# Performance work log

Hardware: AMD Instinct MI355X
Metric: run time of the kernel (lower is better)

The kernel has to match this reference:

```python
import jax, jax.numpy as jnp
import numpy as np

N_NODES = 200000
N_BONDS = 220000
D = 128


def setup_inputs() -> dict:
    key = jax.random.key(0)
    ks = jax.random.split(key, 8)
    h = jax.random.normal(ks[0], (N_NODES, D), dtype=jnp.float32)
    src = jax.random.randint(ks[1], (N_BONDS,), 0, N_NODES, dtype=jnp.int64)
    dst = jax.random.randint(ks[2], (N_BONDS,), 0, N_NODES, dtype=jnp.int64)
    # MLP params (Sequential: Linear(256,128)+ReLU, Linear(128,128)+ReLU, Linear(128,2))
    W1 = jax.random.normal(ks[3], (2 * D, 128), dtype=jnp.float32) * (1.0 / np.sqrt(2 * D))
    b1 = jnp.zeros((128,), dtype=jnp.float32)
    W2 = jax.random.normal(ks[4], (128, 128), dtype=jnp.float32) * (1.0 / np.sqrt(128))
    b2 = jnp.zeros((128,), dtype=jnp.float32)
    W3 = jax.random.normal(ks[5], (128, 2), dtype=jnp.float32) * (1.0 / np.sqrt(128))
    b3 = jnp.zeros((2,), dtype=jnp.float32)
    return {"h": h, "src": src, "dst": dst,
            "W1": W1, "b1": b1, "W2": W2, "b2": b2, "W3": W3, "b3": b3}


def _mlp(x, W1, b1, W2, b2, W3, b3):
    x = jax.nn.relu(x @ W1 + b1)
    x = jax.nn.relu(x @ W2 + b2)
    return x @ W3 + b3


def reference(h, src, dst, W1, b1, W2, b2, W3, b3):
    # forward edges: (src -> dst); reverse edges: (dst -> src)
    h_src = h[src]            # [E, D] gather
    h_dst = h[dst]            # [E, D] gather
    h_forward = jnp.concatenate([h_src, h_dst], axis=1)  # [E, 2D]
    h_reverse = jnp.concatenate([h_dst, h_src], axis=1)  # [E, 2D]
    return (_mlp(h_forward, W1, b1, W2, b2, W3, b3)
            + _mlp(h_reverse, W1, b1, W2, b2, W3, b3))
```

## Files before the change

### kernel.cpp

```cpp
#include <hip/hip_runtime.h>
#include <hip/hip_bf16.h>
#include <stdint.h>


typedef __attribute__((ext_vector_type(8))) short bf16x8;
typedef __attribute__((ext_vector_type(4))) float f32x4;

__device__ __forceinline__ float bf2f(unsigned u16) {
    union { unsigned u; float f; } v; v.u = u16 << 16;
    return v.f;
}
__device__ __forceinline__ unsigned short f2bf(float f) {
    union { float f; unsigned u; } v; v.f = f;
    unsigned u = v.u;
    unsigned r = u + 0x7FFFu + ((u >> 16) & 1u);
    return (unsigned short)(r >> 16);
}

__device__ __forceinline__ int swz(int f, int c) {
    return f * 128 + ((c ^ (f & 7)) << 3);
}
__device__ __forceinline__ int swzA(int f, int c) {
    return f * 256 + ((c ^ (f & 7)) << 3);
}

__device__ __forceinline__ bf16x8 cvt8v(float4 x, float4 y) {
    union { bf16x8 v; __hip_bfloat162 h[4]; } R;
    R.h[0] = __float22bfloat162_rn(float2{x.x, x.y});
    R.h[1] = __float22bfloat162_rn(float2{x.z, x.w});
    R.h[2] = __float22bfloat162_rn(float2{y.x, y.y});
    R.h[3] = __float22bfloat162_rn(float2{y.z, y.w});
    return R.v;
}

#define MFMA(a, b, c) __builtin_amdgcn_mfma_f32_16x16x32_bf16((a), (b), (c), 0, 0, 0)

__global__ void prep_weights(const float* __restrict__ W1,
                             const float* __restrict__ W2,
                             unsigned short* __restrict__ W1c,
                             unsigned short* __restrict__ W2t) {
    int idx = blockIdx.x * 256 + threadIdx.x;
    if (idx < 128 * 256) {
        int j = idx >> 8, k = idx & 255;
        W1c[idx] = f2bf(W1[k * 128 + j]);
    } else {
        int i2 = idx - 128 * 256;
        if (i2 < 128 * 128) {
            int n = i2 >> 7, k = i2 & 127;
            W2t[i2] = f2bf(W2[k * 128 + n]);
        }
    }
}

__global__ __launch_bounds__(512, 1) void edge_fused(
    const float* __restrict__ h, const int* __restrict__ src,
    const int* __restrict__ dst, const unsigned short* __restrict__ W1c,
    const unsigned short* __restrict__ W2t, const float* __restrict__ b1,
    const float* __restrict__ b2, const float* __restrict__ W3,
    const float* __restrict__ b3, float* __restrict__ out, int E) {
    __shared__ unsigned short W1s[128 * 256];
    __shared__ unsigned short W2s[128 * 128];
    __shared__ unsigned short scr[8 * 16 * 128];
    __shared__ float  cb1[128];
    __shared__ float  cb2[128];
    __shared__ float2 cW3[128];

    int t = threadIdx.x;
    int lane = t & 63;
    int wv = t >> 6;
    int ml = lane & 15, quad = lane >> 4;

    {
        int r = t >> 2, q = t & 3;
        const uint4* s = (const uint4*)(W1c + (size_t)r * 256 + q * 64);
#pragma unroll
        for (int i = 0; i < 8; ++i)
            *(uint4*)(W1s + swzA(r, q * 8 + i)) = s[i];
    }
    {
        int f = t >> 2, q4 = t & 3;
        const uint4* s = (const uint4*)(W2t + (size_t)f * 128 + q4 * 32);
#pragma unroll
        for (int i = 0; i < 4; ++i)
            *(uint4*)(W2s + swz(f, q4 * 4 + i)) = s[i];
    }
    if (t < 128) {
        cb1[t] = b1[t];
        cb2[t] = b2[t];
        cW3[t] = float2{W3[t * 2 + 0], W3[t * 2 + 1]};
    }

    int e = blockIdx.x * 128 + wv * 16 + ml;
    int ec = (e < E) ? e : (E - 1);
    int si = src[ec], di = dst[ec];
    const float* hs = h + (size_t)si * 128;
    const float* hd = h + (size_t)di * 128;

    float4 s0a, s0b, s1a, s1b, s2a, s2b, s3a, s3b;
    float4 d0a, d0b, d1a, d1b, d2a, d2b, d3a, d3b;
    {
        int ko = quad * 8;
        s0a = *(const float4*)(hs + ko);       s0b = *(const float4*)(hs + ko + 4);
        s1a = *(const float4*)(hs + 32 + ko);  s1b = *(const float4*)(hs + 36 + ko);
        s2a = *(const float4*)(hs + 64 + ko);  s2b = *(const float4*)(hs + 68 + ko);
        s3a = *(const float4*)(hs + 96 + ko);  s3b = *(const float4*)(hs + 100 + ko);
        d0a = *(const float4*)(hd + ko);       d0b = *(const float4*)(hd + ko + 4);
        d1a = *(const float4*)(hd + 32 + ko);  d1b = *(const float4*)(hd + 36 + ko);
        d2a = *(const float4*)(hd + 64 + ko);  d2b = *(const float4*)(hd + 68 + ko);
        d3a = *(const float4*)(hd + 96 + ko);  d3b = *(const float4*)(hd + 100 + ko);
    }
    bf16x8 hsf[4], hdf[4];
    hsf[0] = cvt8v(s0a, s0b); hsf[1] = cvt8v(s1a, s1b);
    hsf[2] = cvt8v(s2a, s2b); hsf[3] = cvt8v(s3a, s3b);
    hdf[0] = cvt8v(d0a, d0b); hdf[1] = cvt8v(d1a, d1b);
    hdf[2] = cvt8v(d2a, d2b); hdf[3] = cvt8v(d3a, d3b);

    __syncthreads();

    unsigned short* scrW = scr + wv * 2048;
    bf16x8 afw[4], arv[4];

    {
        f32x4 accf[8] = {}, accr[8] = {};
#pragma unroll
        for (int kk = 0; kk < 4; ++kk) {
#pragma unroll
            for (int ct = 0; ct < 8; ++ct) {
                bf16x8 a = *(const bf16x8*)(W1s + swzA(ct * 16 + ml, kk * 4 + quad));
                accf[ct] = MFMA(a, hsf[kk], accf[ct]);
                accr[ct] = MFMA(a, hdf[kk], accr[ct]);
            }
        }
#pragma unroll
        for (int kk = 4; kk < 8; ++kk) {
#pragma unroll
            for (int ct = 0; ct < 8; ++ct) {
                bf16x8 a = *(const bf16x8*)(W1s + swzA(ct * 16 + ml, kk * 4 + quad));
                accf[ct] = MFMA(a, hdf[kk - 4], accf[ct]);
                accr[ct] = MFMA(a, hsf[kk - 4], accr[ct]);
            }
        }

#pragma unroll
        for (int ct = 0; ct < 8; ++ct) {
            int fb = ct * 16 + quad * 4;
            float4 bv = *(const float4*)(cb1 + fb);
            union { uint2 u; __hip_bfloat162 h2[2]; } o;
            o.h2[0] = __float22bfloat162_rn(float2{fmaxf(accf[ct][0] + bv.x, 0.f),
                                                   fmaxf(accf[ct][1] + bv.y, 0.f)});
            o.h2[1] = __float22bfloat162_rn(float2{fmaxf(accf[ct][2] + bv.z, 0.f),
                                                   fmaxf(accf[ct][3] + bv.w, 0.f)});
            int chunk = ct * 2 + (quad >> 1);
            *(uint2*)(scrW + ml * 128 + ((chunk ^ (ml & 7)) << 3) + ((quad & 1) << 2)) = o.u;
        }
        __threadfence_block();
#pragma unroll
        for (int kk = 0; kk < 4; ++kk) {
            int chunk = kk * 4 + quad;
            afw[kk] = *(const bf16x8*)(scrW + ml * 128 + ((chunk ^ (ml & 7)) << 3));
        }
        __threadfence_block();

#pragma unroll
        for (int ct = 0; ct < 8; ++ct) {
            int fb = ct * 16 + quad * 4;
            float4 bv = *(const float4*)(cb1 + fb);
            union { uint2 u; __hip_bfloat162 h2[2]; } o;
            o.h2[0] = __float22bfloat162_rn(float2{fmaxf(accr[ct][0] + bv.x, 0.f),
                                                   fmaxf(accr[ct][1] + bv.y, 0.f)});
            o.h2[1] = __float22bfloat162_rn(float2{fmaxf(accr[ct][2] + bv.z, 0.f),
                                                   fmaxf(accr[ct][3] + bv.w, 0.f)});
            int chunk = ct * 2 + (quad >> 1);
            *(uint2*)(scrW + ml * 128 + ((chunk ^ (ml & 7)) << 3) + ((quad & 1) << 2)) = o.u;
        }
        __threadfence_block();
#pragma unroll
        for (int kk = 0; kk < 4; ++kk) {
            int chunk = kk * 4 + quad;
            arv[kk] = *(const bf16x8*)(scrW + ml * 128 + ((chunk ^ (ml & 7)) << 3));
        }
    }

    float p0[4] = {0.f, 0.f, 0.f, 0.f};
    float p1[4] = {0.f, 0.f, 0.f, 0.f};
    {
        f32x4 acc2f[8] = {}, acc2r[8] = {};
#pragma unroll
        for (int kk = 0; kk < 4; ++kk) {
#pragma unroll
            for (int ct = 0; ct < 8; ++ct) {
                bf16x8 b = *(const bf16x8*)(W2s + swz(ct * 16 + ml, kk * 4 + quad));
                acc2f[ct] = MFMA(afw[kk], b, acc2f[ct]);
                acc2r[ct] = MFMA(arv[kk], b, acc2r[ct]);
            }
        }
#pragma unroll
        for (int ct = 0; ct < 8; ++ct) {
            int c = ct * 16 + ml;
            float2 w3 = cW3[c];
            float bc = cb2[c];
#pragma unroll
            for (int reg = 0; reg < 4; ++reg) {
                float hf = fmaxf(acc2f[ct][reg] + bc, 0.f);
                float hr = fmaxf(acc2r[ct][reg] + bc, 0.f);
                p0[reg] += (hf + hr) * w3.x;
                p1[reg] += (hf + hr) * w3.y;
            }
        }
    }

#pragma unroll
    for (int m = 1; m < 16; m <<= 1) {
#pragma unroll
        for (int reg = 0; reg < 4; ++reg) {
            p0[reg] += __shfl_xor(p0[reg], m);
            p1[reg] += __shfl_xor(p1[reg], m);
        }
    }

    if (ml < 2) {
        float bb = 2.f * b3[ml];
#pragma unroll
        for (int reg = 0; reg < 4; ++reg) {
            int ee = blockIdx.x * 128 + wv * 16 + quad * 4 + reg;
            if (ee < E) {
                float v = (ml == 0) ? p0[reg] : p1[reg];
                out[(size_t)ee * 2 + ml] = v + bb;
            }
        }
    }
}

extern "C" void kernel_launch(void* const* d_in, const int* in_sizes, int n_in,
                              void* d_out, int out_size, void* d_ws, size_t ws_size,
                              hipStream_t stream) {
    (void)n_in; (void)out_size; (void)ws_size;
    const float* h  = (const float*)d_in[0];
    const int*   sr = (const int*)d_in[1];
    const int*   ds = (const int*)d_in[2];
    const float* W1 = (const float*)d_in[3];
    const float* b1 = (const float*)d_in[4];
    const float* W2 = (const float*)d_in[5];
    const float* b2 = (const float*)d_in[6];
    const float* W3 = (const float*)d_in[7];
    const float* b3 = (const float*)d_in[8];
    float* out = (float*)d_out;

    int E = in_sizes[1];

    unsigned short* W1c = (unsigned short*)d_ws;
    unsigned short* W2t = W1c + 128 * 256;

    prep_weights<<<(128 * 256 + 128 * 128 + 255) / 256, 256, 0, stream>>>(W1, W2, W1c, W2t);

    int etiles = (E + 127) / 128;
    edge_fused<<<etiles, 512, 0, stream>>>(h, sr, ds, W1c, W2t, b1, b2, W3, b3, out, E);
}
```

Before: 227.2 us.

## Alias W1, W2 and scratch in one shared region to raise occupancy

Shared memory is cut from about 130KB to 64KB. W1 and W2 now share one region, with a barrier after layer 1 and before W2 is loaded. The per-wave scratch sits in the upper half. Biases and W3 are read straight from global memory instead of LDS. The launch bound rises from 1 to 4 blocks per CU so more blocks can overlap their gather latency. This adds two barriers and serialises W2 loading after layer 1, and the tighter register budget may cause spilling of the large accumulator arrays.

After: 236.8 us. 4.3% more time.

```diff
diff --git a/kernel.cpp b/kernel.cpp
--- a/kernel.cpp
+++ b/kernel.cpp
@@ -52,18 +52,13 @@
     }
 }
 
-__global__ __launch_bounds__(512, 1) void edge_fused(
+__global__ __launch_bounds__(512, 4) void edge_fused(
     const float* __restrict__ h, const int* __restrict__ src,
     const int* __restrict__ dst, const unsigned short* __restrict__ W1c,
     const unsigned short* __restrict__ W2t, const float* __restrict__ b1,
     const float* __restrict__ b2, const float* __restrict__ W3,
     const float* __restrict__ b3, float* __restrict__ out, int E) {
-    __shared__ unsigned short W1s[128 * 256];
-    __shared__ unsigned short W2s[128 * 128];
-    __shared__ unsigned short scr[8 * 16 * 128];
-    __shared__ float  cb1[128];
-    __shared__ float  cb2[128];
-    __shared__ float2 cW3[128];
+    __shared__ unsigned short region[128 * 256];
 
     int t = threadIdx.x;
     int lane = t & 63;
@@ -75,19 +70,7 @@
         const uint4* s = (const uint4*)(W1c + (size_t)r * 256 + q * 64);
 #pragma unroll
         for (int i = 0; i < 8; ++i)
-            *(uint4*)(W1s + swzA(r, q * 8 + i)) = s[i];
-    }
-    {
-        int f = t >> 2, q4 = t & 3;
-        const uint4* s = (const uint4*)(W2t + (size_t)f * 128 + q4 * 32);
-#pragma unroll
-        for (int i = 0; i < 4; ++i)
-            *(uint4*)(W2s + swz(f, q4 * 4 + i)) = s[i];
-    }
-    if (t < 128) {
-        cb1[t] = b1[t];
-        cb2[t] = b2[t];
-        cW3[t] = float2{W3[t * 2 + 0], W3[t * 2 + 1]};
+            *(uint4*)(region + swzA(r, q * 8 + i)) = s[i];
     }
 
     int e = blockIdx.x * 128 + wv * 16 + ml;
@@ -117,34 +100,43 @@
 
     __syncthreads();
 
-    unsigned short* scrW = scr + wv * 2048;
+    f32x4 accf[8] = {}, accr[8] = {};
+#pragma unroll
+    for (int kk = 0; kk < 4; ++kk) {
+#pragma unroll
+        for (int ct = 0; ct < 8; ++ct) {
+            bf16x8 a = *(const bf16x8*)(region + swzA(ct * 16 + ml, kk * 4 + quad));
+            accf[ct] = MFMA(a, hsf[kk], accf[ct]);
+            accr[ct] = MFMA(a, hdf[kk], accr[ct]);
+        }
+    }
+#pragma unroll
+    for (int kk = 4; kk < 8; ++kk) {
+#pragma unroll
+        for (int ct = 0; ct < 8; ++ct) {
+            bf16x8 a = *(const bf16x8*)(region + swzA(ct * 16 + ml, kk * 4 + quad));
+            accf[ct] = MFMA(a, hdf[kk - 4], accf[ct]);
+            accr[ct] = MFMA(a, hsf[kk - 4], accr[ct]);
+        }
+    }
+
+    __syncthreads();
+
+    {
+        int f = t >> 2, q4 = t & 3;
+        const uint4* s = (const uint4*)(W2t + (size_t)f * 128 + q4 * 32);
+#pragma unroll
+        for (int i = 0; i < 4; ++i)
+            *(uint4*)(region + swz(f, q4 * 4 + i)) = s[i];
+    }
+
+    unsigned short* scrW = region + 16384 + wv * 2048;
     bf16x8 afw[4], arv[4];
-
-    {
-        f32x4 accf[8] = {}, accr[8] = {};
-#pragma unroll
-        for (int kk = 0; kk < 4; ++kk) {
-#pragma unroll
-            for (int ct = 0; ct < 8; ++ct) {
-                bf16x8 a = *(const bf16x8*)(W1s + swzA(ct * 16 + ml, kk * 4 + quad));
-                accf[ct] = MFMA(a, hsf[kk], accf[ct]);
-                accr[ct] = MFMA(a, hdf[kk], accr[ct]);
-            }
-        }
-#pragma unroll
-        for (int kk = 4; kk < 8; ++kk) {
-#pragma unroll
-            for (int ct = 0; ct < 8; ++ct) {
-                bf16x8 a = *(const bf16x8*)(W1s + swzA(ct * 16 + ml, kk * 4 + quad));
-                accf[ct] = MFMA(a, hdf[kk - 4], accf[ct]);
-                accr[ct] = MFMA(a, hsf[kk - 4], accr[ct]);
-            }
-        }
-
+    {
 #pragma unroll
         for (int ct = 0; ct < 8; ++ct) {
             int fb = ct * 16 + quad * 4;
-            float4 bv = *(const float4*)(cb1 + fb);
+            float4 bv = *(const float4*)(b1 + fb);
             union { uint2 u; __hip_bfloat162 h2[2]; } o;
             o.h2[0] = __float22bfloat162_rn(float2{fmaxf(accf[ct][0] + bv.x, 0.f),
                                                    fmaxf(accf[ct][1] + bv.y, 0.f)});
@@ -164,7 +156,7 @@
 #pragma unroll
         for (int ct = 0; ct < 8; ++ct) {
             int fb = ct * 16 + quad * 4;
-            float4 bv = *(const float4*)(cb1 + fb);
+            float4 bv = *(const float4*)(b1 + fb);
             union { uint2 u; __hip_bfloat162 h2[2]; } o;
             o.h2[0] = __float22bfloat162_rn(float2{fmaxf(accr[ct][0] + bv.x, 0.f),
                                                    fmaxf(accr[ct][1] + bv.y, 0.f)});
@@ -181,6 +173,8 @@
         }
     }
 
+    __syncthreads();
+
     float p0[4] = {0.f, 0.f, 0.f, 0.f};
     float p1[4] = {0.f, 0.f, 0.f, 0.f};
     {
@@ -189,7 +183,7 @@
         for (int kk = 0; kk < 4; ++kk) {
 #pragma unroll
             for (int ct = 0; ct < 8; ++ct) {
-                bf16x8 b = *(const bf16x8*)(W2s + swz(ct * 16 + ml, kk * 4 + quad));
+                bf16x8 b = *(const bf16x8*)(region + swz(ct * 16 + ml, kk * 4 + quad));
                 acc2f[ct] = MFMA(afw[kk], b, acc2f[ct]);
                 acc2r[ct] = MFMA(arv[kk], b, acc2r[ct]);
             }
@@ -197,8 +191,8 @@
 #pragma unroll
         for (int ct = 0; ct < 8; ++ct) {
             int c = ct * 16 + ml;
-            float2 w3 = cW3[c];
-            float bc = cb2[c];
+            float2 w3 = *(const float2*)(W3 + c * 2);
+            float bc = b2[c];
 #pragma unroll
             for (int reg = 0; reg < 4; ++reg) {
                 float hf = fmaxf(acc2f[ct][reg] + bc, 0.f);
```
